# Kernel tuning notes

Hardware: AMD Instinct MI355X
Metric: run time of the kernel (lower is better)

The kernel has to match this reference:

```python
import jax, jax.numpy as jnp
import numpy as np

B, T = 512, 8192
DT = jnp.float32(1e-3)


def setup_inputs() -> dict:
    key = jax.random.key(0)
    k1, k2, k3, k4 = jax.random.split(key, 4)
    # scale noise so the 8192-step linear recurrence stays well-conditioned
    xicovs = jax.random.normal(k1, (B, T, 2, 2), jnp.float32) * 0.05
    dy = jax.random.normal(k2, (B, T, 2), jnp.float32) * 0.05
    coeffs_A = jax.random.uniform(k3, (2, 2), jnp.float32, -0.05, 0.05)  # 'uniform' init kernel
    C = jax.random.normal(k4, (2, 2), jnp.float32)
    return {"xicovs": xicovs, "dy": dy, "coeffs_A": coeffs_A, "C": C}


def reference(xicovs, dy, coeffs_A, C):
    # xicovs: [B,T,2,2], dy: [B,T,2]
    Bv = xicovs.shape[0]
    # initial state [1,0] broadcast over batch
    x0 = jnp.broadcast_to(jnp.array([1.0, 0.0], jnp.float32), (Bv, 2))
    xi_t = jnp.swapaxes(xicovs, 0, 1)  # [T,B,2,2]
    dy_t = jnp.swapaxes(dy, 0, 1)      # [T,B,2]

    def step(x, inp):
        xic, dyt = inp  # [B,2,2], [B,2]
        # cell emits C @ x_prev * dt
        out = jnp.einsum('ij,bj->bi', C, x) * DT
        A_minus_xiC = coeffs_A - jnp.einsum('bij,jk->bik', xic, C)  # [B,2,2]
        dx = jnp.einsum('bij,bj->bi', A_minus_xiC, x) * DT + jnp.einsum('bij,bj->bi', xic, dyt)
        return x + dx, out

    _, outs = jax.lax.scan(step, x0, (xi_t, dy_t))  # outs: [T,B,2]
    return jnp.swapaxes(outs, 0, 1)  # [B,T,2] (return_sequences=True)
```

## Files before the change

### kernel.cpp

```cpp
#include <hip/hip_runtime.h>


#define B_   512
#define T_   8192
#define LPT  8
#define NT   1024
static_assert(NT * LPT == T_, "one block covers one batch");

struct Aff { float m00, m01, m10, m11, v0, v1; };

__device__ __forceinline__ Aff aff_compose(const Aff& L, const Aff& E) {
    Aff r;
    r.m00 = L.m00*E.m00 + L.m01*E.m10;
    r.m01 = L.m00*E.m01 + L.m01*E.m11;
    r.m10 = L.m10*E.m00 + L.m11*E.m10;
    r.m11 = L.m10*E.m01 + L.m11*E.m11;
    r.v0  = L.m00*E.v0  + L.m01*E.v1 + L.v0;
    r.v1  = L.m10*E.v0  + L.m11*E.v1 + L.v1;
    return r;
}

__device__ __forceinline__ Aff aff_identity() {
    Aff r; r.m00 = 1.f; r.m01 = 0.f; r.m10 = 0.f; r.m11 = 1.f; r.v0 = 0.f; r.v1 = 0.f;
    return r;
}

__global__ __launch_bounds__(NT) void grm_fused(
    const float* __restrict__ xic, const float* __restrict__ dy,
    const float* __restrict__ Aptr, const float* __restrict__ Cptr,
    float4* __restrict__ out4)
{
    __shared__ float wtot[16][6];

    const int b    = blockIdx.x;
    const int tid  = threadIdx.x;
    const int lane = tid & 63;
    const int wave = tid >> 6;

    const float DT = 1e-3f;
    const float c00 = Cptr[0], c01 = Cptr[1], c10 = Cptr[2], c11 = Cptr[3];
    const float cd00 = c00*DT, cd01 = c01*DT, cd10 = c10*DT, cd11 = c11*DT;
    const float i00 = 1.0f + Aptr[0]*DT, i01 = Aptr[1]*DT;
    const float i10 = Aptr[2]*DT,        i11 = 1.0f + Aptr[3]*DT;

    const float4* xv = (const float4*)xic + ((size_t)b * T_ + tid * LPT);
    const float4* dv = (const float4*)dy  + ((size_t)b * T_ + tid * LPT) / 2;

    float4 a[LPT];
    float4 d[LPT/2];
    #pragma unroll
    for (int i = 0; i < LPT; ++i)   a[i] = xv[i];
    #pragma unroll
    for (int i = 0; i < LPT/2; ++i) d[i] = dv[i];

#define STEP_MAP(i, S)                                                  \
    {                                                                   \
        const float4 x4 = a[i];                                         \
        const float dyx = ((i)&1) ? d[(i)>>1].z : d[(i)>>1].x;          \
        const float dyy = ((i)&1) ? d[(i)>>1].w : d[(i)>>1].y;          \
        (S).m00 = i00 - (x4.x*cd00 + x4.y*cd10);                        \
        (S).m01 = i01 - (x4.x*cd01 + x4.y*cd11);                        \
        (S).m10 = i10 - (x4.z*cd00 + x4.w*cd10);                        \
        (S).m11 = i11 - (x4.z*cd01 + x4.w*cd11);                        \
        (S).v0  = x4.x*dyx + x4.y*dyy;                                  \
        (S).v1  = x4.z*dyx + x4.w*dyy;                                  \
    }

    Aff P;
    STEP_MAP(0, P);
    #pragma unroll
    for (int i = 1; i < LPT; ++i) { Aff s; STEP_MAP(i, s); P = aff_compose(s, P); }

    Aff S = P;
    #pragma unroll
    for (int sh = 1; sh < 64; sh <<= 1) {
        Aff q;
        q.m00 = __shfl_up(S.m00, sh); q.m01 = __shfl_up(S.m01, sh);
        q.m10 = __shfl_up(S.m10, sh); q.m11 = __shfl_up(S.m11, sh);
        q.v0  = __shfl_up(S.v0,  sh); q.v1  = __shfl_up(S.v1,  sh);
        if (lane >= sh) S = aff_compose(S, q);
    }

    if (lane == 63) {
        wtot[wave][0] = S.m00; wtot[wave][1] = S.m01;
        wtot[wave][2] = S.m10; wtot[wave][3] = S.m11;
        wtot[wave][4] = S.v0;  wtot[wave][5] = S.v1;
    }
    __syncthreads();

    Aff Ew = aff_identity();
    for (int w = 0; w < wave; ++w) {
        Aff t;
        t.m00 = wtot[w][0]; t.m01 = wtot[w][1];
        t.m10 = wtot[w][2]; t.m11 = wtot[w][3];
        t.v0  = wtot[w][4]; t.v1  = wtot[w][5];
        Ew = aff_compose(t, Ew);
    }

    Aff El;
    El.m00 = __shfl_up(S.m00, 1); El.m01 = __shfl_up(S.m01, 1);
    El.m10 = __shfl_up(S.m10, 1); El.m11 = __shfl_up(S.m11, 1);
    El.v0  = __shfl_up(S.v0,  1); El.v1  = __shfl_up(S.v1,  1);
    if (lane == 0) El = aff_identity();

    Aff E = aff_compose(El, Ew);
    float x0 = E.m00 + E.v0;
    float x1 = E.m10 + E.v1;

    float o[LPT][2];
    #pragma unroll
    for (int i = 0; i < LPT; ++i) {
        o[i][0] = cd00*x0 + cd01*x1;
        o[i][1] = cd10*x0 + cd11*x1;
        Aff s; STEP_MAP(i, s);
        float nx0 = s.m00*x0 + s.m01*x1 + s.v0;
        float nx1 = s.m10*x0 + s.m11*x1 + s.v1;
        x0 = nx0; x1 = nx1;
    }
#undef STEP_MAP

    float4* ov = out4 + ((size_t)b * T_ + tid * LPT) / 2;
    #pragma unroll
    for (int i = 0; i < LPT/2; ++i)
        ov[i] = make_float4(o[2*i][0], o[2*i][1], o[2*i+1][0], o[2*i+1][1]);
}

extern "C" void kernel_launch(void* const* d_in, const int* in_sizes, int n_in,
                              void* d_out, int out_size, void* d_ws, size_t ws_size,
                              hipStream_t stream) {
    const float* xic  = (const float*)d_in[0];
    const float* dy   = (const float*)d_in[1];
    const float* Aptr = (const float*)d_in[2];
    const float* Cptr = (const float*)d_in[3];
    float4* out = (float4*)d_out;

    grm_fused<<<B_, NT, 0, stream>>>(xic, dy, Aptr, Cptr, out);
}
```

Baseline: 147.0 us.

## Coalesce global loads and stores via swizzled LDS transpose per wave

Each wave now loads its contiguous chunk of xicovs and dy with lane-strided float4 accesses, so adjacent lanes read adjacent addresses. The data is then transposed through a 64KB XOR-swizzled LDS buffer into the per-thread 8-step layout. Outputs go back through LDS the same way so the global stores are coalesced too. The change also sets launch_bounds min-blocks to 4 and reuses the LDS slice for the wave totals, which needs an extra barrier. The large LDS allocation may limit how many blocks fit per CU.

```diff
diff --git a/kernel.cpp b/kernel.cpp
--- a/kernel.cpp
+++ b/kernel.cpp
@@ -25,33 +25,65 @@
     return r;
 }
 
-__global__ __launch_bounds__(NT) void grm_fused(
+__global__ __launch_bounds__(NT, 4) void grm_fused(
     const float* __restrict__ xic, const float* __restrict__ dy,
     const float* __restrict__ Aptr, const float* __restrict__ Cptr,
     float4* __restrict__ out4)
 {
-    __shared__ float wtot[16][6];
+    __shared__ float4 lds4[16 * 256];
 
     const int b    = blockIdx.x;
     const int tid  = threadIdx.x;
     const int lane = tid & 63;
     const int wave = tid >> 6;
 
+    float4* slice = lds4 + wave * 256;
+
     const float DT = 1e-3f;
-    const float c00 = Cptr[0], c01 = Cptr[1], c10 = Cptr[2], c11 = Cptr[3];
-    const float cd00 = c00*DT, cd01 = c01*DT, cd10 = c10*DT, cd11 = c11*DT;
+    const float cd00 = Cptr[0]*DT, cd01 = Cptr[1]*DT;
+    const float cd10 = Cptr[2]*DT, cd11 = Cptr[3]*DT;
     const float i00 = 1.0f + Aptr[0]*DT, i01 = Aptr[1]*DT;
     const float i10 = Aptr[2]*DT,        i11 = 1.0f + Aptr[3]*DT;
 
-    const float4* xv = (const float4*)xic + ((size_t)b * T_ + tid * LPT);
-    const float4* dv = (const float4*)dy  + ((size_t)b * T_ + tid * LPT) / 2;
+    const int wbase = b * T_ + wave * 512;
+    const float4* xw = (const float4*)xic + wbase;
+    const float4* dw = (const float4*)dy  + (wbase >> 1);
+    float4*       ow = out4 + (wbase >> 1);
+
+    float4 t[8], u[4];
+    #pragma unroll
+    for (int j = 0; j < 8; ++j) t[j] = xw[j*64 + lane];
+    #pragma unroll
+    for (int j = 0; j < 4; ++j) u[j] = dw[j*64 + lane];
 
     float4 a[LPT];
-    float4 d[LPT/2];
     #pragma unroll
-    for (int i = 0; i < LPT; ++i)   a[i] = xv[i];
+    for (int rr = 0; rr < 2; ++rr) {
+        #pragma unroll
+        for (int jj = 0; jj < 4; ++jj) {
+            int j = 4*rr + jj;
+            int f = j*64 + lane;
+            int rel = (f >> 3) & 31;
+            slice[rel*8 + ((lane & 7) ^ (rel & 7))] = t[j];
+        }
+        if ((lane >> 5) == rr) {
+            int rel = lane & 31;
+            #pragma unroll
+            for (int s = 0; s < LPT; ++s)
+                a[s] = slice[rel*8 + (s ^ (rel & 7))];
+        }
+    }
+
     #pragma unroll
-    for (int i = 0; i < LPT/2; ++i) d[i] = dv[i];
+    for (int j = 0; j < 4; ++j) {
+        int f = j*64 + lane;
+        int o = f >> 2;
+        slice[o*4 + ((lane & 3) ^ (o & 3))] = u[j];
+    }
+    float4 d[4];
+    #pragma unroll
+    for (int s = 0; s < 4; ++s)
+        d[s] = slice[lane*4 + (s ^ (lane & 3))];
 
 #define STEP_MAP(i, S)                                                  \
     {                                                                   \
@@ -82,20 +114,21 @@
     }
 
     if (lane == 63) {
-        wtot[wave][0] = S.m00; wtot[wave][1] = S.m01;
-        wtot[wave][2] = S.m10; wtot[wave][3] = S.m11;
-        wtot[wave][4] = S.v0;  wtot[wave][5] = S.v1;
+        float* h = (float*)slice;
+        h[0] = S.m00; h[1] = S.m01; h[2] = S.m10; h[3] = S.m11;
+        h[4] = S.v0;  h[5] = S.v1;
     }
     __syncthreads();
 
     Aff Ew = aff_identity();
     for (int w = 0; w < wave; ++w) {
-        Aff t;
-        t.m00 = wtot[w][0]; t.m01 = wtot[w][1];
-        t.m10 = wtot[w][2]; t.m11 = wtot[w][3];
-        t.v0  = wtot[w][4]; t.v1  = wtot[w][5];
-        Ew = aff_compose(t, Ew);
+        const float* h = (const float*)(lds4 + w * 256);
+        Aff t2;
+        t2.m00 = h[0]; t2.m01 = h[1]; t2.m10 = h[2]; t2.m11 = h[3];
+        t2.v0  = h[4]; t2.v1  = h[5];
+        Ew = aff_compose(t2, Ew);
     }
+    __syncthreads();
 
     Aff El;
     El.m00 = __shfl_up(S.m00, 1); El.m01 = __shfl_up(S.m01, 1);
@@ -107,11 +140,13 @@
     float x0 = E.m00 + E.v0;
     float x1 = E.m10 + E.v1;
 
-    float o[LPT][2];
+    float4 o4[4];
     #pragma unroll
     for (int i = 0; i < LPT; ++i) {
-        o[i][0] = cd00*x0 + cd01*x1;
-        o[i][1] = cd10*x0 + cd11*x1;
+        float oxx = cd00*x0 + cd01*x1;
+        float oyy = cd10*x0 + cd11*x1;
+        if (i & 1) { o4[i>>1].z = oxx; o4[i>>1].w = oyy; }
+        else       { o4[i>>1].x = oxx; o4[i>>1].y = oyy; }
         Aff s; STEP_MAP(i, s);
         float nx0 = s.m00*x0 + s.m01*x1 + s.v0;
         float nx1 = s.m10*x0 + s.m11*x1 + s.v1;
@@ -119,10 +154,15 @@
     }
 #undef STEP_MAP
 
-    float4* ov = out4 + ((size_t)b * T_ + tid * LPT) / 2;
     #pragma unroll
-    for (int i = 0; i < LPT/2; ++i)
-        ov[i] = make_float4(o[2*i][0], o[2*i][1], o[2*i+1][0], o[2*i+1][1]);
+    for (int s = 0; s < 4; ++s)
+        slice[lane*4 + (s ^ (lane & 3))] = o4[s];
+    #pragma unroll
+    for (int j = 0; j < 4; ++j) {
+        int f = j*64 + lane;
+        int o = f >> 2;
+        ow[f] = slice[o*4 + ((lane & 3) ^ (o & 3))];
+    }
 }
 
 extern "C" void kernel_launch(void* const* d_in, const int* in_sizes, int n_in,
```

Result: faster. 140.4 us (-4.5%).
